# Performance work log

Measured on AMD Instinct MI355X. Metric: run time of the kernel, lower is better.

## Reference

```python
import jax, jax.numpy as jnp
import numpy as np

B, T, IN = 256, 100, 784
H = 200            # LSTM cell size
R = 4              # read heads
N, D = 128, 40     # memory rows x memory dim
NCLASS = 5
GAMMA = 0.95


def setup_inputs() -> dict:
    key = jax.random.key(0)
    ks = jax.random.split(key, 9)
    s = 0.05

    def lin(k, out_dim, in_dim):
        k1, k2 = jax.random.split(k)
        return (jax.random.normal(k1, (out_dim, in_dim), jnp.float32) * s,
                jax.random.normal(k2, (out_dim,), jnp.float32) * s)

    Wkey, bkey = lin(ks[0], R * D, H)
    Wadd, badd = lin(ks[1], R * D, H)
    Wsig, bsig = lin(ks[2], 1, H)
    Who, bho = lin(ks[3], NCLASS, H)
    Wro, bro = lin(ks[4], NCLASS, R * D)
    Wrh, brh = lin(ks[5], H, R * D)
    Wih, bih = lin(ks[6], 4 * H, IN)
    Whh, bhh = lin(ks[7], 4 * H, H)
    x = jax.random.normal(ks[8], (B, T, IN), jnp.float32)
    return dict(x=x, Wkey=Wkey, bkey=bkey, Wadd=Wadd, badd=badd,
                Wsig=Wsig, bsig=bsig, Who=Who, bho=bho, Wro=Wro, bro=bro,
                Wrh=Wrh, brh=brh, Wih=Wih, bih=bih, Whh=Whh, bhh=bhh)


def _cosine(x, y, eps=1e-6):
    # x: [B,R,D], y: [B,N,D] -> [B,R,N]
    z = jnp.einsum('brd,bnd->brn', x, y)
    x2 = jnp.sum(x * x, axis=-1)[:, :, None]
    y2 = jnp.sum(y * y, axis=-1)[:, None, :]
    return z / jnp.sqrt(x2 * y2 + eps)


def _mann_forward(x, Wkey, bkey, Wadd, badd, Wsig, bsig, Who, bho, Wro, bro,
                  Wrh, brh, Wih, bih, Whh, bhh):
    bs = x.shape[0]
    batch_idx = jnp.arange(bs)[:, None]

    def step(carry, x_t):
        M, wr, wu, c, h, r = carry
        # inject read vector into hidden state
        h = h + r @ Wrh.T + brh
        # LSTMCell (torch gate order: i, f, g, o)
        gates = x_t @ Wih.T + bih + h @ Whh.T + bhh
        i_g, f_g, g_g, o_g = jnp.split(gates, 4, axis=-1)
        i_g = jax.nn.sigmoid(i_g)
        f_g = jax.nn.sigmoid(f_g)
        g_g = jnp.tanh(g_g)
        o_g = jax.nn.sigmoid(o_g)
        c_t = f_g * c + i_g * g_g
        h_t = o_g * jnp.tanh(c_t)

        key = (h_t @ Wkey.T + bkey).reshape(bs, R, D)
        add = (h_t @ Wadd.T + badd).reshape(bs, R, D)
        sigma = h_t @ Wsig.T + bsig            # [B,1] (raw linear, as in source)

        # least-used one-hot mask (no grad through it)
        wu_sg = jax.lax.stop_gradient(wu)
        lu_idx = jnp.argsort(wu_sg, axis=1)[:, :R]          # [B,R]
        wlu = jnp.zeros((bs, N), x_t.dtype).at[batch_idx, lu_idx].set(1.0)

        sig = sigma[:, :, None]                              # [B,1,1]
        ww = sig * wr + (1.0 - sig) * wlu[:, None, :]        # [B,R,N]
        M_t = M * wlu[:, :, None] + jnp.einsum('brn,brd->bnd', ww, add)

        K = _cosine(key, M_t)                                # [B,R,N]
        wr_t = jax.nn.softmax(K, axis=-1)
        wu_t = GAMMA * wu + wr_t.sum(axis=1) + ww.sum(axis=1)
        r_t = jnp.einsum('brn,bnd->brd', wr_t, M_t).reshape(bs, R * D)

        out_t = h_t @ Who.T + bho + r_t @ Wro.T + bro        # [B,NCLASS]
        return (M_t, wr_t, wu_t, c_t, h_t, r_t), out_t

    init = (jnp.zeros((bs, N, D), x.dtype),
            jnp.zeros((bs, R, N), x.dtype),
            jnp.zeros((bs, N), x.dtype),
            jnp.zeros((bs, H), x.dtype),
            jnp.zeros((bs, H), x.dtype),
            jnp.zeros((bs, R * D), x.dtype))
    _, outs = jax.lax.scan(step, init, jnp.transpose(x, (1, 0, 2)))
    return jnp.transpose(outs, (1, 0, 2))  # [B,T,NCLASS]


def reference(x, Wkey, bkey, Wadd, badd, Wsig, bsig, Who, bho, Wro, bro,
              Wrh, brh, Wih, bih, Whh, bhh):
    return _mann_forward(x, Wkey, bkey, Wadd, badd, Wsig, bsig, Who, bho,
                         Wro, bro, Wrh, brh, Wih, bih, Whh, bhh)
```

## Files before the change

kernel.cpp:

```cpp
#include <hip/hip_runtime.h>
#include <math.h>

#define TB   100
#define BB   256
#define INF_ 784
#define HH   200
#define RR   4
#define NN   128
#define DD   40
#define NCLS 5
#define G4H  800
#define KAW  324
#define MST  44

typedef __attribute__((ext_vector_type(8))) short bf16x8;
typedef __attribute__((ext_vector_type(4))) float f32x4;

__device__ __forceinline__ float sigmoidf_(float x) { return 1.0f / (1.0f + expf(-x)); }

__device__ __forceinline__ void splitbf_(float v, unsigned short &hi, unsigned short &lo) {
  const unsigned b = __float_as_uint(v);
  hi = (unsigned short)(b >> 16);
  const float hf = __uint_as_float(b & 0xFFFF0000u);
  lo = (unsigned short)(__float_as_uint(v - hf) >> 16);
}

__device__ __forceinline__ unsigned short bf16rne_(float v) {
  const unsigned u = __float_as_uint(v);
  return (unsigned short)((u + 0x7FFFu + ((u >> 16) & 1u)) >> 16);
}

#define ADV(c, CC) { ++(c); if ((c) == (CC)) (c) = 0; }

#define PIPE4(CC, OFS, LOADM, FMAM)                                     \
  {                                                                     \
    int chL = (OFS), chF = (OFS);                                       \
    LOADM(w0, chL); ADV(chL, CC); LOADM(w1, chL); ADV(chL, CC);         \
    LOADM(w2, chL); ADV(chL, CC);                                       \
    _Pragma("unroll 1")                                                 \
    for (int g = 0; g < ((CC) - 3) / 4; ++g) {                          \
      LOADM(w3, chL); ADV(chL, CC); FMAM(w0, chF); ADV(chF, CC);        \
      LOADM(w0, chL); ADV(chL, CC); FMAM(w1, chF); ADV(chF, CC);        \
      LOADM(w1, chL); ADV(chL, CC); FMAM(w2, chF); ADV(chF, CC);        \
      LOADM(w2, chL); ADV(chL, CC); FMAM(w3, chF); ADV(chF, CC);        \
    }                                                                   \
    {                                                                   \
      constexpr int REMX = (CC) - 3 - 4 * (((CC) - 3) / 4);             \
      if (REMX >= 1) { LOADM(w3, chL); ADV(chL, CC); }                  \
      FMAM(w0, chF); ADV(chF, CC);                                      \
      if (REMX >= 2) { LOADM(w0, chL); ADV(chL, CC); }                  \
      FMAM(w1, chF); ADV(chF, CC);                                      \
      if (REMX >= 3) { LOADM(w1, chL); ADV(chL, CC); }                  \
      FMAM(w2, chF); ADV(chF, CC);                                      \
      if (REMX >= 1) { FMAM(w3, chF); ADV(chF, CC); }                   \
      if (REMX >= 2) { FMAM(w0, chF); ADV(chF, CC); }                   \
      if (REMX >= 3) { FMAM(w1, chF); ADV(chF, CC); }                   \
    }                                                                   \
  }

#define BFUP(V, WE, WO)                                                  \
  const float WE = __uint_as_float((unsigned)(V) << 16);                 \
  const float WO = __uint_as_float((unsigned)(V) & 0xFFFF0000u);

__global__ __launch_bounds__(256) void prep_kernel(
    const float* __restrict__ Whh, const float* __restrict__ Wrh,
    const float* __restrict__ Wkey, const float* __restrict__ Wadd,
    const float* __restrict__ Wsig, const float* __restrict__ bkey,
    const float* __restrict__ badd, const float* __restrict__ bsig,
    unsigned short* __restrict__ WhhP, unsigned short* __restrict__ WrhP,
    unsigned short* __restrict__ WkaP, float* __restrict__ bka)
{
  const int tid = blockIdx.x * 256 + threadIdx.x;
  if (tid < 160000) {
    const int j = tid / 200, k = tid - j * 200;
    WhhP[(k >> 1) * 1600 + j * 2 + (k & 1)] = bf16rne_(Whh[tid]);
  }
  if (tid < 32000) {
    const int j = tid / 160, m = tid - j * 160;
    WrhP[(m >> 1) * 400 + j * 2 + (m & 1)] = bf16rne_(Wrh[tid]);
  }
  if (tid < 200 * KAW) {
    const int k = tid / KAW, j = tid - k * KAW;
    float v = 0.0f;
    if (j < 160)       v = Wkey[j * HH + k];
    else if (j < 320)  v = Wadd[(j - 160) * HH + k];
    else if (j == 320) v = Wsig[k];
    WkaP[(k >> 1) * (2 * KAW) + j * 2 + (k & 1)] = bf16rne_(v);
  }
  if (tid < KAW) {
    float v = 0.0f;
    if (tid < 160)       v = bkey[tid];
    else if (tid < 320)  v = badd[tid - 160];
    else if (tid == 320) v = bsig[0];
    bka[tid] = v;
  }
}

#define GM  128
#define GN  80
#define LDK 40

__global__ __launch_bounds__(256) void gemm_in2_kernel(
    const float* __restrict__ X, const float* __restrict__ Wih,
    const float* __restrict__ bih, const float* __restrict__ bhh,
    float* __restrict__ G)
{
  __shared__ __attribute__((aligned(16))) unsigned short Ahi[GM][LDK];
  __shared__ __attribute__((aligned(16))) unsigned short Alo[GM][LDK];
  __shared__ __attribute__((aligned(16))) unsigned short Bhi[GN][LDK];
  __shared__ __attribute__((aligned(16))) unsigned short Blo[GN][LDK];

  const int tid  = threadIdx.x;
  const int wv   = tid >> 6, lane = tid & 63;
  const int n0   = blockIdx.x * GN;
  const int m0   = blockIdx.y * GM;

  f32x4 acc[2][5];
#pragma unroll
  for (int mt = 0; mt < 2; ++mt)
#pragma unroll
    for (int nt = 0; nt < 5; ++nt) acc[mt][nt] = (f32x4){0.f, 0.f, 0.f, 0.f};

  const int arow = tid >> 1, ak = (tid & 1) * 16;
  const float* Ap = X + (size_t)(m0 + arow) * INF_ + ak;
  const float* Bp = Wih + (size_t)(n0 + arow) * INF_ + ak;

  const int fr = lane & 15, fk = (lane >> 4) * 8;

  for (int kk = 0; kk < 800; kk += 32) {
    float va[16], vb[16];
    const bool av = (kk + ak) < INF_;
#pragma unroll
    for (int i = 0; i < 16; ++i) va[i] = 0.f;
    if (av) {
      *(float4*)&va[0]  = *(const float4*)(Ap + kk);
      *(float4*)&va[4]  = *(const float4*)(Ap + kk + 4);
      *(float4*)&va[8]  = *(const float4*)(Ap + kk + 8);
      *(float4*)&va[12] = *(const float4*)(Ap + kk + 12);
    }
    if (tid < 160) {
#pragma unroll
      for (int i = 0; i < 16; ++i) vb[i] = 0.f;
      if (av) {
        *(float4*)&vb[0]  = *(const float4*)(Bp + kk);
        *(float4*)&vb[4]  = *(const float4*)(Bp + kk + 4);
        *(float4*)&vb[8]  = *(const float4*)(Bp + kk + 8);
        *(float4*)&vb[12] = *(const float4*)(Bp + kk + 12);
      }
    }
    __syncthreads();
    {
      unsigned ah[8], al[8];
#pragma unroll
      for (int i = 0; i < 8; ++i) {
        unsigned short h0, l0, h1, l1;
        splitbf_(va[2 * i], h0, l0);
        splitbf_(va[2 * i + 1], h1, l1);
        ah[i] = (unsigned)h0 | ((unsigned)h1 << 16);
        al[i] = (unsigned)l0 | ((unsigned)l1 << 16);
      }
      ((int4*)&Ahi[arow][ak])[0] = make_int4(ah[0], ah[1], ah[2], ah[3]);
      ((int4*)&Ahi[arow][ak + 8])[0] = make_int4(ah[4], ah[5], ah[6], ah[7]);
      ((int4*)&Alo[arow][ak])[0] = make_int4(al[0], al[1], al[2], al[3]);
      ((int4*)&Alo[arow][ak + 8])[0] = make_int4(al[4], al[5], al[6], al[7]);
    }
    if (tid < 160) {
      unsigned bh[8], bl[8];
#pragma unroll
      for (int i = 0; i < 8; ++i) {
        unsigned short h0, l0, h1, l1;
        splitbf_(vb[2 * i], h0, l0);
        splitbf_(vb[2 * i + 1], h1, l1);
        bh[i] = (unsigned)h0 | ((unsigned)h1 << 16);
        bl[i] = (unsigned)l0 | ((unsigned)l1 << 16);
      }
      ((int4*)&Bhi[arow][ak])[0] = make_int4(bh[0], bh[1], bh[2], bh[3]);
      ((int4*)&Bhi[arow][ak + 8])[0] = make_int4(bh[4], bh[5], bh[6], bh[7]);
      ((int4*)&Blo[arow][ak])[0] = make_int4(bl[0], bl[1], bl[2], bl[3]);
      ((int4*)&Blo[arow][ak + 8])[0] = make_int4(bl[4], bl[5], bl[6], bl[7]);
    }
    __syncthreads();
    const bf16x8 a0h = *(const bf16x8*)&Ahi[wv * 32 + fr][fk];
    const bf16x8 a0l = *(const bf16x8*)&Alo[wv * 32 + fr][fk];
    const bf16x8 a1h = *(const bf16x8*)&Ahi[wv * 32 + 16 + fr][fk];
    const bf16x8 a1l = *(const bf16x8*)&Alo[wv * 32 + 16 + fr][fk];
#pragma unroll
    for (int nt = 0; nt < 5; ++nt) {
      const bf16x8 bh = *(const bf16x8*)&Bhi[nt * 16 + fr][fk];
      const bf16x8 bl = *(const bf16x8*)&Blo[nt * 16 + fr][fk];
      acc[0][nt] = __builtin_amdgcn_mfma_f32_16x16x32_bf16(a0h, bh, acc[0][nt], 0, 0, 0);
      acc[1][nt] = __builtin_amdgcn_mfma_f32_16x16x32_bf16(a1h, bh, acc[1][nt], 0, 0, 0);
      acc[0][nt] = __builtin_amdgcn_mfma_f32_16x16x32_bf16(a0l, bh, acc[0][nt], 0, 0, 0);
      acc[1][nt] = __builtin_amdgcn_mfma_f32_16x16x32_bf16(a1l, bh, acc[1][nt], 0, 0, 0);
      acc[0][nt] = __builtin_amdgcn_mfma_f32_16x16x32_bf16(a0h, bl, acc[0][nt], 0, 0, 0);
      acc[1][nt] = __builtin_amdgcn_mfma_f32_16x16x32_bf16(a1h, bl, acc[1][nt], 0, 0, 0);
    }
  }

#pragma unroll
  for (int nt = 0; nt < 5; ++nt) {
    const int en = n0 + nt * 16 + fr;
    const float bs = bih[en] + bhh[en];
#pragma unroll
    for (int mt = 0; mt < 2; ++mt) {
      const int emb = m0 + wv * 32 + mt * 16 + (lane >> 4) * 4;
#pragma unroll
      for (int r = 0; r < 4; ++r)
        G[(size_t)(emb + r) * G4H + en] = acc[mt][nt][r] + bs;
    }
  }
}

__global__ __launch_bounds__(512, 2) void mann_kernel(
    const float* __restrict__ G, const unsigned short* __restrict__ WhhP,
    const unsigned short* __restrict__ WrhP, const unsigned short* __restrict__ WkaP,
    const float* __restrict__ bka, const float* __restrict__ brh,
    const float* __restrict__ Who, const float* __restrict__ bho,
    const float* __restrict__ Wro, const float* __restrict__ bro,
    float* __restrict__ out)
{
  __shared__ __attribute__((aligned(16))) float M_s[NN * MST];
  __shared__ __attribute__((aligned(16))) float h_s[HH];
  __shared__ __attribute__((aligned(16))) float c_s[HH];
  __shared__ __attribute__((aligned(16))) float r_s[RR * DD];
  __shared__ __attribute__((aligned(16))) float brh_s[HH];
  __shared__ float wr_s[RR * NN];
  __shared__ float ww_s[RR * NN];
  __shared__ float wu_s[NN];
  __shared__ float Mn2_s[NN];
  __shared__ float kn2_s[RR];
  __shared__ __attribute__((aligned(16))) float gates_s[G4H];
  __shared__ __attribute__((aligned(16))) float ka_s[KAW];
  __shared__ __attribute__((aligned(16))) float bka_s[KAW];
  __shared__ __attribute__((aligned(16))) float Gbuf_s[G4H];
  __shared__ float Who_s[NCLS * HH], Wro_s[NCLS * RR * DD], bo_s[NCLS];
  __shared__ int   lu_s[RR];

  float*  Kp   = &gates_s[0];
  float4* pkA4 = (float4*)&gates_s[0];
  float4* pka4 = (float4*)&gates_s[0];

  const int tid = threadIdx.x;
  const int b   = blockIdx.x;

  for (int e = tid; e < NN * MST; e += 512) M_s[e] = 0.f;
  if (tid < RR * NN) wr_s[tid] = 0.f;
  if (tid < NN) wu_s[tid] = 0.f;
  if (tid < HH) { h_s[tid] = 0.f; c_s[tid] = 0.f; brh_s[tid] = brh[tid]; }
  if (tid < RR * DD) r_s[tid] = 0.f;
  if (tid < KAW) bka_s[tid] = bka[tid];
  for (int e = tid; e < NCLS * HH; e += 512) Who_s[e] = Who[e];
  for (int e = tid; e < NCLS * RR * DD; e += 512) Wro_s[e] = Wro[e];
  if (tid < NCLS) bo_s[tid] = bho[tid] + bro[tid];
  if (tid < 200)
    ((float4*)Gbuf_s)[tid] = ((const float4*)(G + (size_t)b * TB * G4H))[tid];
  __syncthreads();

  const int ofs1 = (int)((blockIdx.x * 3u) % 8u);
  const int ofs2 = (int)((blockIdx.x * 7u) % 20u);
  const int ofs4 = (int)((blockIdx.x * 3u) % 10u);

#pragma clang loop unroll(disable)
  for (int t = 0; t < TB; ++t) {
    float4 a0v = make_float4(0.f, 0.f, 0.f, 0.f);

    if (tid < 100) {
      const int kh = tid / 50, j4 = tid - kh * 50;
      const int k2beg = kh * 40;
      const int4* __restrict__ Wr4 = (const int4*)WrhP + (size_t)k2beg * 50 + j4;
      int4 w0[5], w1[5], w2[5], w3[5];
#define P1_LOAD(B, CH) { const int mm = (CH) * 5; _Pragma("unroll") \
      for (int u = 0; u < 5; ++u) B[u] = Wr4[(mm + u) * 50]; }
#define P1_FMA(B, CH) { const int kc = k2beg + (CH) * 5; _Pragma("unroll") \
      for (int u = 0; u < 5; ++u) { \
        const float2 rk = *(const float2*)&r_s[(kc + u) * 2]; \
        BFUP(B[u].x, we0, wo0) BFUP(B[u].y, we1, wo1) \
        BFUP(B[u].z, we2, wo2) BFUP(B[u].w, we3, wo3) \
        a0v.x += rk.x * we0 + rk.y * wo0; \
        a0v.y += rk.x * we1 + rk.y * wo1; \
        a0v.z += rk.x * we2 + rk.y * wo2; \
        a0v.w += rk.x * we3 + rk.y * wo3; } }
      PIPE4(8, ofs1, P1_LOAD, P1_FMA)
      if (kh) pkA4[j4] = a0v;
    }
    __syncthreads();
    if (tid < 50) {
      const float4 pA = pkA4[tid];
      const float4 brv = ((const float4*)brh_s)[tid];
      float4 hv = *(const float4*)&h_s[4 * tid];
      hv.x += brv.x + a0v.x + pA.x;
      hv.y += brv.y + a0v.y + pA.y;
      hv.z += brv.z + a0v.z + pA.z;
      hv.w += brv.w + a0v.w + pA.w;
      *(float4*)&h_s[4 * tid] = hv;
    }
    __syncthreads();

    if (tid < 200) {
      const int4* __restrict__ Wh4 = (const int4*)WhhP + tid;
      float4 g0 = *(const float4*)&Gbuf_s[4 * tid];
      int4 w0[5], w1[5], w2[5], w3[5];
#define P2_LOAD(B, CH) { const int kk = (CH) * 5; _Pragma("unroll") \
      for (int u = 0; u < 5; ++u) B[u] = Wh4[(kk + u) * 200]; }
#define P2_FMA(B, CH) { const int kc = (CH) * 5; _Pragma("unroll") \
      for (int u = 0; u < 5; ++u) { \
        const float2 hk = *(const float2*)&h_s[(kc + u) * 2]; \
        BFUP(B[u].x, we0, wo0) BFUP(B[u].y, we1, wo1) \
        BFUP(B[u].z, we2, wo2) BFUP(B[u].w, we3, wo3) \
        g0.x += hk.x * we0 + hk.y * wo0; \
        g0.y += hk.x * we1 + hk.y * wo1; \
        g0.z += hk.x * we2 + hk.y * wo2; \
        g0.w += hk.x * we3 + hk.y * wo3; } }
      PIPE4(20, ofs2, P2_LOAD, P2_FMA)
      *(float4*)&gates_s[4 * tid] = g0;
    }
    __syncthreads();

    if (tid < HH) {
      const float ig = sigmoidf_(gates_s[tid]);
      const float fg = sigmoidf_(gates_s[HH + tid]);
      const float gg = tanhf(gates_s[2 * HH + tid]);
      const float og = sigmoidf_(gates_s[3 * HH + tid]);
      const float cn = fg * c_s[tid] + ig * gg;
      c_s[tid] = cn;
      h_s[tid] = og * tanhf(cn);
    }
    __syncthreads();

    float4 kav0 = make_float4(0.f, 0.f, 0.f, 0.f);
    if (tid < 162) {
      const int kh = tid / 81, j4 = tid - kh * 81;
      const int k2beg = kh * 50;
      const int4* __restrict__ Wk4 = (const int4*)WkaP + (size_t)k2beg * 81 + j4;
      int4 w0[5], w1[5], w2[5], w3[5];
#define P4_LOAD(B, CH) { const int kk = (CH) * 5; _Pragma("unroll") \
      for (int u = 0; u < 5; ++u) B[u] = Wk4[(kk + u) * 81]; }
#define P4_FMA(B, CH) { const int kc = k2beg + (CH) * 5; _Pragma("unroll") \
      for (int u = 0; u < 5; ++u) { \
        const float2 hk = *(const float2*)&h_s[(kc + u) * 2]; \
        BFUP(B[u].x, we0, wo0) BFUP(B[u].y, we1, wo1) \
        BFUP(B[u].z, we2, wo2) BFUP(B[u].w, we3, wo3) \
        kav0.x += hk.x * we0 + hk.y * wo0; \
        kav0.y += hk.x * we1 + hk.y * wo1; \
        kav0.z += hk.x * we2 + hk.y * wo2; \
        kav0.w += hk.x * we3 + hk.y * wo3; } }
      PIPE4(10, ofs4, P4_LOAD, P4_FMA)
      if (kh) pka4[j4] = kav0;
    } else if (tid >= 384 && t + 1 < TB) {
      for (int idx = tid - 384; idx < 200; idx += 128)
        ((float4*)Gbuf_s)[idx] =
            ((const float4*)(G + ((size_t)b * TB + t + 1) * G4H))[idx];
    }
    __syncthreads();
    if (tid < 81) {
      const float4 bbv = ((const float4*)bka_s)[tid];
      const float4 p0 = pka4[tid];
      float4 v0;
      v0.x = kav0.x + p0.x + bbv.x; v0.y = kav0.y + p0.y + bbv.y;
      v0.z = kav0.z + p0.z + bbv.z; v0.w = kav0.w + p0.w + bbv.w;
      *(float4*)&ka_s[4 * tid] = v0;
    }
    __syncthreads();

    if (tid < 64) {
      const int l = tid;
      unsigned u0v = __float_as_uint(wu_s[l]);
      unsigned u1v = __float_as_uint(wu_s[l + 64]);
      if (u0v == 0x80000000u) u0v = 0u;
      if (u1v == 0x80000000u) u1v = 0u;
      u0v = (u0v & 0x80000000u) ? ~u0v : (u0v | 0x80000000u);
      u1v = (u1v & 0x80000000u) ? ~u1v : (u1v | 0x80000000u);
      unsigned long long k0 = ((unsigned long long)u0v << 32) | (unsigned)l;
      unsigned long long k1 = ((unsigned long long)u1v << 32) | (unsigned)(l + 64);
#pragma unroll
      for (int rsel = 0; rsel < RR; ++rsel) {
        unsigned long long mn = (k0 < k1) ? k0 : k1;
#pragma unroll
        for (int off = 32; off; off >>= 1) {
          const unsigned long long o = __shfl_xor(mn, off);
          if (o < mn) mn = o;
        }
        const int idx = (int)(mn & 0xFFFFFFFFull);
        if (l == 0) lu_s[rsel] = idx;
        if (idx == l)      k0 = ~0ull;
        if (idx == l + 64) k1 = ~0ull;
      }
    } else if (tid < 68) {
      const int q = tid - 64;
      float s = 0.f;
#pragma unroll
      for (int d4 = 0; d4 < 10; ++d4) {
        const float4 v = *(const float4*)&ka_s[q * DD + 4 * d4];
        s += v.x * v.x + v.y * v.y + v.z * v.z + v.w * v.w;
      }
      kn2_s[q] = s;
    }
    __syncthreads();

    if (tid < NN) {
      const int n = tid;
      const int l0 = lu_s[0], l1 = lu_s[1], l2 = lu_s[2], l3 = lu_s[3];
      const float wlu = (n == l0 || n == l1 || n == l2 || n == l3) ? 1.f : 0.f;
      const float sg = ka_s[320];
      const float oms = (1.f - sg) * wlu;
      const float wwv0 = sg * wr_s[n]          + oms;
      const float wwv1 = sg * wr_s[NN + n]     + oms;
      const float wwv2 = sg * wr_s[2 * NN + n] + oms;
      const float wwv3 = sg * wr_s[3 * NN + n] + oms;
      ww_s[n]          = wwv0;
      ww_s[NN + n]     = wwv1;
      ww_s[2 * NN + n] = wwv2;
      ww_s[3 * NN + n] = wwv3;
      float* Mr = &M_s[n * MST];
      const float* Ad = &ka_s[160];
      float mn2 = 0.f;
#pragma unroll
      for (int d4 = 0; d4 < 10; ++d4) {
        float4 m = *(const float4*)&Mr[4 * d4];
        m.x *= wlu; m.y *= wlu; m.z *= wlu; m.w *= wlu;
        const float4 av0 = *(const float4*)&Ad[0 * DD + 4 * d4];
        const float4 av1 = *(const float4*)&Ad[1 * DD + 4 * d4];
        const float4 av2 = *(const float4*)&Ad[2 * DD + 4 * d4];
        const float4 av3 = *(const float4*)&Ad[3 * DD + 4 * d4];
        m.x += wwv0 * av0.x + wwv1 * av1.x + wwv2 * av2.x + wwv3 * av3.x;
        m.y += wwv0 * av0.y + wwv1 * av1.y + wwv2 * av2.y + wwv3 * av3.y;
        m.z += wwv0 * av0.z + wwv1 * av1.z + wwv2 * av2.z + wwv3 * av3.z;
        m.w += wwv0 * av0.w + wwv1 * av1.w + wwv2 * av2.w + wwv3 * av3.w;
        *(float4*)&Mr[4 * d4] = m;
        mn2 += m.x * m.x + m.y * m.y + m.z * m.z + m.w * m.w;
      }
      Mn2_s[n] = mn2;
    }
    __syncthreads();

    {
      const int q = tid >> 7, n = tid & (NN - 1);
      const float* Mr = &M_s[n * MST];
      const float* Ky = &ka_s[q * DD];
      float s = 0.f;
#pragma unroll
      for (int d4 = 0; d4 < 10; ++d4) {
        const float4 mv = *(const float4*)&Mr[4 * d4];
        const float4 kv = *(const float4*)&Ky[4 * d4];
        s += kv.x * mv.x + kv.y * mv.y + kv.z * mv.z + kv.w * mv.w;
      }
      Kp[q * NN + n] = s / sqrtf(kn2_s[q] * Mn2_s[n] + 1e-6f);
    }
    __syncthreads();

    {
      const int w = tid >> 6, l = tid & 63;
      if (w < 4) {
        float* Kr = Kp + w * NN;
        const float v0 = Kr[l], v1 = Kr[l + 64];
        float mx = fmaxf(v0, v1);
#pragma unroll
        for (int off = 32; off; off >>= 1) mx = fmaxf(mx, __shfl_xor(mx, off));
        const float e0 = expf(v0 - mx), e1 = expf(v1 - mx);
        float s = e0 + e1;
#pragma unroll
        for (int off = 32; off; off >>= 1) s += __shfl_xor(s, off);
        const float inv = 1.f / s;
        Kr[l] = e0 * inv; Kr[l + 64] = e1 * inv;
      }
    }
    __syncthreads();

    if (tid < 320) {
      const int g = tid >> 3, ns = tid & 7;
      const int q = g / 10, d4 = g - q * 10;
      const float* Kr = Kp + q * NN;
      const float* Mb = &M_s[4 * d4];
      float4 acc = make_float4(0.f, 0.f, 0.f, 0.f);
#pragma unroll
      for (int j = 0; j < 16; ++j) {
        const int n = ns + 8 * j;
        const float kw = Kr[n];
        const float4 mv = *(const float4*)&Mb[n * MST];
        acc.x += kw * mv.x; acc.y += kw * mv.y;
        acc.z += kw * mv.z; acc.w += kw * mv.w;
      }
#pragma unroll
      for (int off = 4; off; off >>= 1) {
        acc.x += __shfl_xor(acc.x, off);
        acc.y += __shfl_xor(acc.y, off);
        acc.z += __shfl_xor(acc.z, off);
        acc.w += __shfl_xor(acc.w, off);
      }
      if (ns == 0) *(float4*)&r_s[q * DD + 4 * d4] = acc;
    } else if (tid < 448) {
      const int n = tid - 320;
      if (n < NN) {
        float s = 0.95f * wu_s[n];
#pragma unroll
        for (int q = 0; q < RR; ++q)
          s += Kp[q * NN + n] + ww_s[q * NN + n];
        wu_s[n] = s;
      }
    }
    __syncthreads();

    if (tid < 64) {
      const size_t ob = ((size_t)b * TB + t) * NCLS;
#pragma unroll
      for (int j = 0; j < NCLS; ++j) {
        float p = 0.f;
        for (int k = tid; k < HH; k += 64)      p += h_s[k] * Who_s[j * HH + k];
        for (int m = tid; m < RR * DD; m += 64) p += r_s[m] * Wro_s[j * RR * DD + m];
#pragma unroll
        for (int off = 32; off; off >>= 1) p += __shfl_xor(p, off);
        if (tid == 0) out[ob + j] = p + bo_s[j];
      }
    } else if (tid >= 256) {
      for (int f = tid - 256; f < RR * NN; f += 256) wr_s[f] = Kp[f];
    }
    __syncthreads();
  }
}

extern "C" void kernel_launch(void* const* d_in, const int* in_sizes, int n_in,
                              void* d_out, int out_size, void* d_ws, size_t ws_size,
                              hipStream_t stream) {
  const float* x    = (const float*)d_in[0];
  const float* Wkey = (const float*)d_in[1];
  const float* bkey = (const float*)d_in[2];
  const float* Wadd = (const float*)d_in[3];
  const float* badd = (const float*)d_in[4];
  const float* Wsig = (const float*)d_in[5];
  const float* bsig = (const float*)d_in[6];
  const float* Who  = (const float*)d_in[7];
  const float* bho  = (const float*)d_in[8];
  const float* Wro  = (const float*)d_in[9];
  const float* bro  = (const float*)d_in[10];
  const float* Wrh  = (const float*)d_in[11];
  const float* brh  = (const float*)d_in[12];
  const float* Wih  = (const float*)d_in[13];
  const float* bih  = (const float*)d_in[14];
  const float* Whh  = (const float*)d_in[15];
  const float* bhh  = (const float*)d_in[16];

  float* ws = (float*)d_ws;
  float* G  = ws;
  unsigned short* WhhP = (unsigned short*)(G + (size_t)25600 * 800);
  unsigned short* WrhP = WhhP + 160000;
  unsigned short* WkaP = WrhP + 32000;
  float* bka = G + (size_t)25600 * 800 + 128400;

  prep_kernel<<<(160000 + 255) / 256, 256, 0, stream>>>(
      Whh, Wrh, Wkey, Wadd, Wsig, bkey, badd, bsig, WhhP, WrhP, WkaP, bka);

  dim3 gA(G4H / GN, 25600 / GM);
  gemm_in2_kernel<<<gA, 256, 0, stream>>>(x, Wih, bih, bhh, G);

  mann_kernel<<<BB, 512, 0, stream>>>(G, WhhP, WrhP, WkaP, bka, brh,
                                      Who, bho, Wro, bro, (float*)d_out);
}
```

Baseline: 2.185 ms.

## Fold Wrh into Whh and overlap next-step Whh·h with the memory stages

Precomputes the product Whh·Wrh and Whh·brh in the prep kernel, so the read vector feeds the gates directly through a 800x160 matrix. This removes the separate r→h projection phase and two barriers per step. The Whh·h_t term for the next step is computed by otherwise idle threads 256-455, in slices spread across the memory-update, cosine and softmax stages. The cosine, read and usage phases are remapped onto fewer threads to free those lanes. The risks are extra bf16 rounding in the combined matrix, higher register pressure in the overlap threads, and a costlier prep kernel.

Result: faster. 1.972 ms (-9.8%).

```diff
diff --git a/kernel.cpp b/kernel.cpp
--- a/kernel.cpp
+++ b/kernel.cpp
@@ -67,17 +67,15 @@
     const float* __restrict__ Wkey, const float* __restrict__ Wadd,
     const float* __restrict__ Wsig, const float* __restrict__ bkey,
     const float* __restrict__ badd, const float* __restrict__ bsig,
-    unsigned short* __restrict__ WhhP, unsigned short* __restrict__ WrhP,
-    unsigned short* __restrict__ WkaP, float* __restrict__ bka)
+    const float* __restrict__ brh,
+    unsigned short* __restrict__ WhhP, unsigned short* __restrict__ WkaP,
+    unsigned short* __restrict__ WcP, float* __restrict__ bka,
+    float* __restrict__ bc)
 {
   const int tid = blockIdx.x * 256 + threadIdx.x;
   if (tid < 160000) {
     const int j = tid / 200, k = tid - j * 200;
     WhhP[(k >> 1) * 1600 + j * 2 + (k & 1)] = bf16rne_(Whh[tid]);
-  }
-  if (tid < 32000) {
-    const int j = tid / 160, m = tid - j * 160;
-    WrhP[(m >> 1) * 400 + j * 2 + (m & 1)] = bf16rne_(Wrh[tid]);
   }
   if (tid < 200 * KAW) {
     const int k = tid / KAW, j = tid - k * KAW;
@@ -86,6 +84,21 @@
     else if (j < 320)  v = Wadd[(j - 160) * HH + k];
     else if (j == 320) v = Wsig[k];
     WkaP[(k >> 1) * (2 * KAW) + j * 2 + (k & 1)] = bf16rne_(v);
+  }
+  if (tid < 128000) {
+    const int j = tid / 160, k = tid - j * 160;
+    const float* wrow = Whh + (size_t)j * 200;
+    float s = 0.f;
+#pragma unroll 4
+    for (int m = 0; m < 200; ++m) s += wrow[m] * Wrh[(size_t)m * 160 + k];
+    WcP[(k >> 1) * 1600 + j * 2 + (k & 1)] = bf16rne_(s);
+  }
+  if (tid < 800) {
+    const float* wrow = Whh + (size_t)tid * 200;
+    float s = 0.f;
+#pragma unroll 4
+    for (int m = 0; m < 200; ++m) s += wrow[m] * brh[m];
+    bc[tid] = s;
   }
   if (tid < KAW) {
     float v = 0.0f;
@@ -213,8 +226,8 @@
 
 __global__ __launch_bounds__(512, 2) void mann_kernel(
     const float* __restrict__ G, const unsigned short* __restrict__ WhhP,
-    const unsigned short* __restrict__ WrhP, const unsigned short* __restrict__ WkaP,
-    const float* __restrict__ bka, const float* __restrict__ brh,
+    const unsigned short* __restrict__ WkaP, const unsigned short* __restrict__ WcP,
+    const float* __restrict__ bka, const float* __restrict__ bc,
     const float* __restrict__ Who, const float* __restrict__ bho,
     const float* __restrict__ Wro, const float* __restrict__ bro,
     float* __restrict__ out)
@@ -223,95 +236,94 @@
   __shared__ __attribute__((aligned(16))) float h_s[HH];
   __shared__ __attribute__((aligned(16))) float c_s[HH];
   __shared__ __attribute__((aligned(16))) float r_s[RR * DD];
-  __shared__ __attribute__((aligned(16))) float brh_s[HH];
   __shared__ float wr_s[RR * NN];
   __shared__ float ww_s[RR * NN];
   __shared__ float wu_s[NN];
   __shared__ float Mn2_s[NN];
   __shared__ float kn2_s[RR];
   __shared__ __attribute__((aligned(16))) float gates_s[G4H];
+  __shared__ __attribute__((aligned(16))) float Kp_s[RR * NN];
   __shared__ __attribute__((aligned(16))) float ka_s[KAW];
   __shared__ __attribute__((aligned(16))) float bka_s[KAW];
-  __shared__ __attribute__((aligned(16))) float Gbuf_s[G4H];
+  __shared__ __attribute__((aligned(16))) float bc_s[G4H];
+  __shared__ __attribute__((aligned(16))) float pka_s[81 * 4];
   __shared__ float Who_s[NCLS * HH], Wro_s[NCLS * RR * DD], bo_s[NCLS];
   __shared__ int   lu_s[RR];
 
-  float*  Kp   = &gates_s[0];
-  float4* pkA4 = (float4*)&gates_s[0];
-  float4* pka4 = (float4*)&gates_s[0];
-
   const int tid = threadIdx.x;
   const int b   = blockIdx.x;
+  const int jl  = tid - 256;
 
   for (int e = tid; e < NN * MST; e += 512) M_s[e] = 0.f;
-  if (tid < RR * NN) wr_s[tid] = 0.f;
+  if (tid < RR * NN) { wr_s[tid] = 0.f; }
   if (tid < NN) wu_s[tid] = 0.f;
-  if (tid < HH) { h_s[tid] = 0.f; c_s[tid] = 0.f; brh_s[tid] = brh[tid]; }
+  if (tid < HH) { h_s[tid] = 0.f; c_s[tid] = 0.f; }
   if (tid < RR * DD) r_s[tid] = 0.f;
   if (tid < KAW) bka_s[tid] = bka[tid];
   for (int e = tid; e < NCLS * HH; e += 512) Who_s[e] = Who[e];
   for (int e = tid; e < NCLS * RR * DD; e += 512) Wro_s[e] = Wro[e];
   if (tid < NCLS) bo_s[tid] = bho[tid] + bro[tid];
-  if (tid < 200)
-    ((float4*)Gbuf_s)[tid] = ((const float4*)(G + (size_t)b * TB * G4H))[tid];
+  if (tid < 200) {
+    ((float4*)bc_s)[tid] = ((const float4*)bc)[tid];
+    const float4 gv = ((const float4*)(G + (size_t)b * TB * G4H))[tid];
+    const float4 bcv = ((const float4*)bc)[tid];
+    *(float4*)&gates_s[4 * tid] =
+        make_float4(gv.x + bcv.x, gv.y + bcv.y, gv.z + bcv.z, gv.w + bcv.w);
+  }
   __syncthreads();
 
-  const int ofs1 = (int)((blockIdx.x * 3u) % 8u);
+  const int ofsc = (int)((blockIdx.x * 5u) % 16u);
   const int ofs2 = (int)((blockIdx.x * 7u) % 20u);
   const int ofs4 = (int)((blockIdx.x * 3u) % 10u);
 
+  const int4* __restrict__ Wh4o = (const int4*)WhhP + ((jl >= 0 && jl < 200) ? jl : 0);
+
+#define OVL_SEG(NCH)                                                  \
+  else if (jl >= 0 && jl < 200) {                                     \
+    _Pragma("unroll")                                                 \
+    for (int s = 0; s < (NCH); ++s) {                                 \
+      int c2 = ochF + ofs2; if (c2 >= 20) c2 -= 20;                   \
+      const int4* __restrict__ pp = Wh4o + (size_t)(c2 * 5) * 200;    \
+      int4 vv[5];                                                     \
+      _Pragma("unroll")                                               \
+      for (int u = 0; u < 5; ++u) vv[u] = pp[u * 200];                \
+      const int kc0 = c2 * 5;                                         \
+      _Pragma("unroll")                                               \
+      for (int u = 0; u < 5; ++u) {                                   \
+        const float2 hk = *(const float2*)&h_s[(kc0 + u) * 2];        \
+        BFUP(vv[u].x, we0, wo0) BFUP(vv[u].y, we1, wo1)               \
+        BFUP(vv[u].z, we2, wo2) BFUP(vv[u].w, we3, wo3)               \
+        oacc.x += hk.x * we0 + hk.y * wo0;                            \
+        oacc.y += hk.x * we1 + hk.y * wo1;                            \
+        oacc.z += hk.x * we2 + hk.y * wo2;                            \
+        oacc.w += hk.x * we3 + hk.y * wo3;                            \
+      }                                                               \
+      ++ochF;                                                         \
+    }                                                                 \
+  }
+
 #pragma clang loop unroll(disable)
   for (int t = 0; t < TB; ++t) {
-    float4 a0v = make_float4(0.f, 0.f, 0.f, 0.f);
-
-    if (tid < 100) {
-      const int kh = tid / 50, j4 = tid - kh * 50;
-      const int k2beg = kh * 40;
-      const int4* __restrict__ Wr4 = (const int4*)WrhP + (size_t)k2beg * 50 + j4;
+    float4 oacc = make_float4(0.f, 0.f, 0.f, 0.f);
+    int ochF = 0;
+    float4 g0 = make_float4(0.f, 0.f, 0.f, 0.f);
+
+    if (tid < 200) {
+      const int4* __restrict__ Wc4 = (const int4*)WcP + tid;
+      g0 = *(const float4*)&gates_s[4 * tid];
       int4 w0[5], w1[5], w2[5], w3[5];
-#define P1_LOAD(B, CH) { const int mm = (CH) * 5; _Pragma("unroll") \
-      for (int u = 0; u < 5; ++u) B[u] = Wr4[(mm + u) * 50]; }
-#define P1_FMA(B, CH) { const int kc = k2beg + (CH) * 5; _Pragma("unroll") \
+#define PA_LOAD(B, CH) { const int kk = (CH) * 5; _Pragma("unroll") \
+      for (int u = 0; u < 5; ++u) B[u] = Wc4[(kk + u) * 200]; }
+#define PA_FMA(B, CH) { const int kc = (CH) * 5; _Pragma("unroll") \
       for (int u = 0; u < 5; ++u) { \
         const float2 rk = *(const float2*)&r_s[(kc + u) * 2]; \
         BFUP(B[u].x, we0, wo0) BFUP(B[u].y, we1, wo1) \
         BFUP(B[u].z, we2, wo2) BFUP(B[u].w, we3, wo3) \
-        a0v.x += rk.x * we0 + rk.y * wo0; \
-        a0v.y += rk.x * we1 + rk.y * wo1; \
-        a0v.z += rk.x * we2 + rk.y * wo2; \
-        a0v.w += rk.x * we3 + rk.y * wo3; } }
-      PIPE4(8, ofs1, P1_LOAD, P1_FMA)
-      if (kh) pkA4[j4] = a0v;
-    }
-    __syncthreads();
-    if (tid < 50) {
-      const float4 pA = pkA4[tid];
-      const float4 brv = ((const float4*)brh_s)[tid];
-      float4 hv = *(const float4*)&h_s[4 * tid];
-      hv.x += brv.x + a0v.x + pA.x;
-      hv.y += brv.y + a0v.y + pA.y;
-      hv.z += brv.z + a0v.z + pA.z;
-      hv.w += brv.w + a0v.w + pA.w;
-      *(float4*)&h_s[4 * tid] = hv;
-    }
-    __syncthreads();
-
-    if (tid < 200) {
-      const int4* __restrict__ Wh4 = (const int4*)WhhP + tid;
-      float4 g0 = *(const float4*)&Gbuf_s[4 * tid];
-      int4 w0[5], w1[5], w2[5], w3[5];
-#define P2_LOAD(B, CH) { const int kk = (CH) * 5; _Pragma("unroll") \
-      for (int u = 0; u < 5; ++u) B[u] = Wh4[(kk + u) * 200]; }
-#define P2_FMA(B, CH) { const int kc = (CH) * 5; _Pragma("unroll") \
-      for (int u = 0; u < 5; ++u) { \
-        const float2 hk = *(const float2*)&h_s[(kc + u) * 2]; \
-        BFUP(B[u].x, we0, wo0) BFUP(B[u].y, we1, wo1) \
-        BFUP(B[u].z, we2, wo2) BFUP(B[u].w, we3, wo3) \
-        g0.x += hk.x * we0 + hk.y * wo0; \
-        g0.y += hk.x * we1 + hk.y * wo1; \
-        g0.z += hk.x * we2 + hk.y * wo2; \
-        g0.w += hk.x * we3 + hk.y * wo3; } }
-      PIPE4(20, ofs2, P2_LOAD, P2_FMA)
+        g0.x += rk.x * we0 + rk.y * wo0; \
+        g0.y += rk.x * we1 + rk.y * wo1; \
+        g0.z += rk.x * we2 + rk.y * wo2; \
+        g0.w += rk.x * we3 + rk.y * wo3; } }
+      PIPE4(16, ofsc, PA_LOAD, PA_FMA)
       *(float4*)&gates_s[4 * tid] = g0;
     }
     __syncthreads();
@@ -345,21 +357,45 @@
         kav0.z += hk.x * we2 + hk.y * wo2; \
         kav0.w += hk.x * we3 + hk.y * wo3; } }
       PIPE4(10, ofs4, P4_LOAD, P4_FMA)
-      if (kh) pka4[j4] = kav0;
-    } else if (tid >= 384 && t + 1 < TB) {
-      for (int idx = tid - 384; idx < 200; idx += 128)
-        ((float4*)Gbuf_s)[idx] =
-            ((const float4*)(G + ((size_t)b * TB + t + 1) * G4H))[idx];
-    }
-    __syncthreads();
+      if (kh) ((float4*)pka_s)[j4] = kav0;
+    }
+    else if (jl >= 0 && jl < 200) {
+      const int tn = (t + 1 < TB) ? t + 1 : t;
+      const float4 gv = *((const float4*)(G + ((size_t)b * TB + tn) * G4H) + jl);
+      const float4 bcv = ((const float4*)bc_s)[jl];
+      oacc = make_float4(gv.x + bcv.x, gv.y + bcv.y, gv.z + bcv.z, gv.w + bcv.w);
+      _Pragma("unroll")
+      for (int s = 0; s < 3; ++s) {
+        int c2 = ochF + ofs2; if (c2 >= 20) c2 -= 20;
+        const int4* __restrict__ pp = Wh4o + (size_t)(c2 * 5) * 200;
+        int4 vv[5];
+        _Pragma("unroll")
+        for (int u = 0; u < 5; ++u) vv[u] = pp[u * 200];
+        const int kc0 = c2 * 5;
+        _Pragma("unroll")
+        for (int u = 0; u < 5; ++u) {
+          const float2 hk = *(const float2*)&h_s[(kc0 + u) * 2];
+          BFUP(vv[u].x, we0, wo0) BFUP(vv[u].y, we1, wo1)
+          BFUP(vv[u].z, we2, wo2) BFUP(vv[u].w, we3, wo3)
+          oacc.x += hk.x * we0 + hk.y * wo0;
+          oacc.y += hk.x * we1 + hk.y * wo1;
+          oacc.z += hk.x * we2 + hk.y * wo2;
+          oacc.w += hk.x * we3 + hk.y * wo3;
+        }
+        ++ochF;
+      }
+    }
+    __syncthreads();
+
     if (tid < 81) {
       const float4 bbv = ((const float4*)bka_s)[tid];
-      const float4 p0 = pka4[tid];
+      const float4 p0 = ((const float4*)pka_s)[tid];
       float4 v0;
       v0.x = kav0.x + p0.x + bbv.x; v0.y = kav0.y + p0.y + bbv.y;
       v0.z = kav0.z + p0.z + bbv.z; v0.w = kav0.w + p0.w + bbv.w;
       *(float4*)&ka_s[4 * tid] = v0;
     }
+    OVL_SEG(3)
     __syncthreads();
 
     if (tid < 64) {
@@ -395,6 +431,7 @@
       }
       kn2_s[q] = s;
     }
+    OVL_SEG(3)
     __syncthreads();
 
     if (tid < NN) {
@@ -431,73 +468,79 @@
       }
       Mn2_s[n] = mn2;
     }
-    __syncthreads();
-
-    {
-      const int q = tid >> 7, n = tid & (NN - 1);
+    OVL_SEG(3)
+    __syncthreads();
+
+    if (tid < 256) {
+      const int qq = tid >> 7, n = tid & (NN - 1);
       const float* Mr = &M_s[n * MST];
-      const float* Ky = &ka_s[q * DD];
-      float s = 0.f;
+      const float* Ky0 = &ka_s[qq * DD];
+      const float* Ky1 = &ka_s[(qq + 2) * DD];
+      float s0 = 0.f, s1 = 0.f;
 #pragma unroll
       for (int d4 = 0; d4 < 10; ++d4) {
         const float4 mv = *(const float4*)&Mr[4 * d4];
-        const float4 kv = *(const float4*)&Ky[4 * d4];
-        s += kv.x * mv.x + kv.y * mv.y + kv.z * mv.z + kv.w * mv.w;
-      }
-      Kp[q * NN + n] = s / sqrtf(kn2_s[q] * Mn2_s[n] + 1e-6f);
-    }
-    __syncthreads();
-
-    {
+        const float4 k0v = *(const float4*)&Ky0[4 * d4];
+        const float4 k1v = *(const float4*)&Ky1[4 * d4];
+        s0 += k0v.x * mv.x + k0v.y * mv.y + k0v.z * mv.z + k0v.w * mv.w;
+        s1 += k1v.x * mv.x + k1v.y * mv.y + k1v.z * mv.z + k1v.w * mv.w;
+      }
+      const float mn2 = Mn2_s[n];
+      Kp_s[qq * NN + n]       = s0 / sqrtf(kn2_s[qq] * mn2 + 1e-6f);
+      Kp_s[(qq + 2) * NN + n] = s1 / sqrtf(kn2_s[qq + 2] * mn2 + 1e-6f);
+    }
+    OVL_SEG(3)
+    __syncthreads();
+
+    if (tid < 256) {
       const int w = tid >> 6, l = tid & 63;
-      if (w < 4) {
-        float* Kr = Kp + w * NN;
-        const float v0 = Kr[l], v1 = Kr[l + 64];
-        float mx = fmaxf(v0, v1);
-#pragma unroll
-        for (int off = 32; off; off >>= 1) mx = fmaxf(mx, __shfl_xor(mx, off));
-        const float e0 = expf(v0 - mx), e1 = expf(v1 - mx);
-        float s = e0 + e1;
-#pragma unroll
-        for (int off = 32; off; off >>= 1) s += __shfl_xor(s, off);
-        const float inv = 1.f / s;
-        Kr[l] = e0 * inv; Kr[l + 64] = e1 * inv;
-      }
-    }
-    __syncthreads();
-
-    if (tid < 320) {
-      const int g = tid >> 3, ns = tid & 7;
+      float* Kr = Kp_s + w * NN;
+      const float v0 = Kr[l], v1 = Kr[l + 64];
+      float mx = fmaxf(v0, v1);
+#pragma unroll
+      for (int off = 32; off; off >>= 1) mx = fmaxf(mx, __shfl_xor(mx, off));
+      const float e0 = expf(v0 - mx), e1 = expf(v1 - mx);
+      float s = e0 + e1;
+#pragma unroll
+      for (int off = 32; off; off >>= 1) s += __shfl_xor(s, off);
+      const float inv = 1.f / s;
+      Kr[l] = e0 * inv; Kr[l + 64] = e1 * inv;
+    }
+    OVL_SEG(3)
+    __syncthreads();
+
+    if (tid < 160) {
+      const int g = tid >> 2, ns = tid & 3;
       const int q = g / 10, d4 = g - q * 10;
-      const float* Kr = Kp + q * NN;
+      const float* Kr = Kp_s + q * NN;
       const float* Mb = &M_s[4 * d4];
       float4 acc = make_float4(0.f, 0.f, 0.f, 0.f);
 #pragma unroll
-      for (int j = 0; j < 16; ++j) {
-        const int n = ns + 8 * j;
+      for (int j = 0; j < 32; ++j) {
+        const int n = ns + 4 * j;
         const float kw = Kr[n];
         const float4 mv = *(const float4*)&Mb[n * MST];
         acc.x += kw * mv.x; acc.y += kw * mv.y;
         acc.z += kw * mv.z; acc.w += kw * mv.w;
       }
 #pragma unroll
-      for (int off = 4; off; off >>= 1) {
+      for (int off = 2; off; off >>= 1) {
         acc.x += __shfl_xor(acc.x, off);
         acc.y += __shfl_xor(acc.y, off);
         acc.z += __shfl_xor(acc.z, off);
         acc.w += __shfl_xor(acc.w, off);
       }
       if (ns == 0) *(float4*)&r_s[q * DD + 4 * d4] = acc;
-    } else if (tid < 448) {
-      const int n = tid - 320;
-      if (n < NN) {
+    } else if (tid < 256) {
+      for (int n = tid - 160; n < NN; n += 96) {
         float s = 0.95f * wu_s[n];
 #pragma unroll
         for (int q = 0; q < RR; ++q)
-          s += Kp[q * NN + n] + ww_s[q * NN + n];
+          s += Kp_s[q * NN + n] + ww_s[q * NN + n];
         wu_s[n] = s;
       }
     }
+    OVL_SEG(2)
     __syncthreads();
 
     if (tid < 64) {
@@ -511,8 +554,10 @@
         for (int off = 32; off; off >>= 1) p += __shfl_xor(p, off);
         if (tid == 0) out[ob + j] = p + bo_s[j];
       }
-    } else if (tid >= 256) {
-      for (int f = tid - 256; f < RR * NN; f += 256) wr_s[f] = Kp[f];
+    } else if (tid < 256) {
+      for (int f = tid - 64; f < RR * NN; f += 192) wr_s[f] = Kp_s[f];
+    } else if (jl < 200) {
+      *(float4*)&gates_s[4 * jl] = oacc;
     }
     __syncthreads();
   }
@@ -542,16 +587,18 @@
   float* ws = (float*)d_ws;
   float* G  = ws;
   unsigned short* WhhP = (unsigned short*)(G + (size_t)25600 * 800);
-  unsigned short* WrhP = WhhP + 160000;
-  unsigned short* WkaP = WrhP + 32000;
-  float* bka = G + (size_t)25600 * 800 + 128400;
+  unsigned short* WkaP = WhhP + 160000;
+  unsigned short* WcP  = WkaP + 64800;
+  float* bka = G + (size_t)25600 * 800 + 176400;
+  float* bc  = bka + 324;
 
   prep_kernel<<<(160000 + 255) / 256, 256, 0, stream>>>(
-      Whh, Wrh, Wkey, Wadd, Wsig, bkey, badd, bsig, WhhP, WrhP, WkaP, bka);
+      Whh, Wrh, Wkey, Wadd, Wsig, bkey, badd, bsig, brh,
+      WhhP, WkaP, WcP, bka, bc);
 
   dim3 gA(G4H / GN, 25600 / GM);
   gemm_in2_kernel<<<gA, 256, 0, stream>>>(x, Wih, bih, bhh, G);
 
-  mann_kernel<<<BB, 512, 0, stream>>>(G, WhhP, WrhP, WkaP, bka, brh,
+  mann_kernel<<<BB, 512, 0, stream>>>(G, WhhP, WkaP, WcP, bka, bc,
                                       Who, bho, Wro, bro, (float*)d_out);
 }
```
